# Optimization experiments

Hardware: AMD Instinct MI355X
Metric: run time of the kernel (lower is better)

The kernel has to match this reference:

```python
import jax, jax.numpy as jnp
import jax.scipy.linalg as jsl
import numpy as np

B, T, C = 2, 4096, 1024
HK = HV = 8           # linear_num_key_heads == linear_num_value_heads
DK = DV = 128         # linear_key_head_dim / linear_value_head_dim
CHUNK = 64
CONV_K = 4
KEY_DIM = HK * DK
VAL_DIM = HV * DV
CONV_DIM = 2 * KEY_DIM + VAL_DIM
EPS = 1e-6


def setup_inputs() -> dict:
    key = jax.random.key(0)
    ks = jax.random.split(key, 8)
    s = 0.02
    x = jax.random.normal(ks[0], (B, T, C), jnp.float32)
    W_qkvz = jax.random.normal(ks[1], (C, 2 * KEY_DIM + 2 * VAL_DIM), jnp.float32) * s
    W_ba = jax.random.normal(ks[2], (C, 2 * HV), jnp.float32) * s
    conv_w = jax.random.normal(ks[3], (CONV_DIM, 1, CONV_K), jnp.float32) * 0.3  # depthwise (O,1,K)
    dt_bias = jnp.ones((HV,), jnp.float32)
    A_log = jnp.log(jax.random.uniform(ks[4], (HV,), jnp.float32, 0.5, 8.0))
    norm_weight = jnp.ones((DV,), jnp.float32)
    W_out = jax.random.normal(ks[5], (VAL_DIM, C), jnp.float32) * s
    return {"x": x, "W_qkvz": W_qkvz, "W_ba": W_ba, "conv_w": conv_w,
            "dt_bias": dt_bias, "A_log": A_log, "norm_weight": norm_weight, "W_out": W_out}


def _l2norm(x, eps=EPS):
    return x * jax.lax.rsqrt(jnp.sum(x * x, -1, keepdims=True) + eps)


def _chunk_gated_delta_rule(q, k, v, g, beta, chunk=CHUNK):
    # q,k: (B,T,H,DK); v: (B,T,H,DV); g,beta: (B,T,H)
    q = _l2norm(q)
    k = _l2norm(k)
    tr = lambda x: jnp.swapaxes(x, 1, 2).astype(jnp.float32)  # -> (B,H,T,...)
    q, k, v, g, beta = tr(q), tr(k), tr(v), tr(g), tr(beta)
    b, h, t, dk = k.shape
    dv = v.shape[-1]
    n = t // chunk  # T divisible by chunk (pad_size == 0)
    q = q * (dk ** -0.5)
    v_beta = v * beta[..., None]
    k_beta = k * beta[..., None]
    rs = lambda x: x.reshape(b, h, n, chunk, x.shape[-1])
    q, k, v_beta, k_beta = rs(q), rs(k), rs(v_beta), rs(k_beta)
    g = jnp.cumsum(g.reshape(b, h, n, chunk), axis=-1)
    # decay_mask[..., i, j] = exp(g_i - g_j) for j <= i, else 0
    decay = jnp.tril(jnp.exp(jnp.tril(g[..., :, None] - g[..., None, :])))
    # forward substitution == unit-lower-triangular solve: (I + tri)^{-1}
    tri = jnp.tril(jnp.einsum('bhnck,bhndk->bhncd', k_beta, k) * decay, -1)
    eye = jnp.eye(chunk, dtype=jnp.float32)
    Tm = jsl.solve_triangular(eye + tri, jnp.broadcast_to(eye, tri.shape), lower=True)
    v_new = Tm @ v_beta                                   # (B,H,N,C,DV)
    k_cum = Tm @ (k_beta * jnp.exp(g)[..., None])         # (B,H,N,C,DK)
    keep_low = jnp.tril(jnp.ones((chunk, chunk), bool))

    def step(S, inp):
        q_i, k_i, v_i, kc_i, g_i, dm_i = inp              # (B,H,C,*)
        attn = jnp.where(keep_low, (q_i @ jnp.swapaxes(k_i, -1, -2)) * dm_i, 0.0)
        v_n = v_i - kc_i @ S
        out = (q_i * jnp.exp(g_i)[..., None]) @ S + attn @ v_n
        g_last = g_i[..., -1]
        S = S * jnp.exp(g_last)[..., None, None] + jnp.einsum(
            'bhck,bhcv->bhkv', k_i * jnp.exp(g_last[..., None] - g_i)[..., None], v_n)
        return S, out

    mv = lambda x: jnp.moveaxis(x, 2, 0)                  # chunk axis to front
    S0 = jnp.zeros((b, h, dk, dv), jnp.float32)
    S, outs = jax.lax.scan(step, S0, (mv(q), mv(k), mv(v_new), mv(k_cum), mv(g), mv(decay)))
    out = jnp.moveaxis(outs, 0, 2).reshape(b, h, t, dv)
    return jnp.swapaxes(out, 1, 2), S                     # (B,T,H,DV), (B,H,DK,DV)


def reference(x, W_qkvz, W_ba, conv_w, dt_bias, A_log, norm_weight, W_out):
    Bx, Tx, Cx = x.shape
    ratio = HV // HK
    qkvz = (x @ W_qkvz).reshape(Bx, Tx, HK, 2 * DK + 2 * ratio * DV)
    q, k, v, z = jnp.split(qkvz, [DK, 2 * DK, 2 * DK + ratio * DV], axis=3)
    v = v.reshape(Bx, Tx, HV, DV)
    z = z.reshape(Bx, Tx, HV, DV)
    ba = (x @ W_ba).reshape(Bx, Tx, HK, 2 * ratio)
    b_, a_ = jnp.split(ba, [ratio], axis=3)
    b_ = b_.reshape(Bx, Tx, HV)
    a_ = a_.reshape(Bx, Tx, HV)
    mixed = jnp.concatenate([q.reshape(Bx, Tx, -1), k.reshape(Bx, Tx, -1),
                             v.reshape(Bx, Tx, -1)], axis=-1)
    # causal depthwise conv1d (left pad K-1, take first T)
    xc = jnp.swapaxes(mixed, 1, 2)                        # (B, CONV_DIM, T)
    conv = jax.lax.conv_general_dilated(xc, conv_w, (1,), [(CONV_K - 1, 0)],
                                        dimension_numbers=('NCH', 'OIH', 'NCH'),
                                        feature_group_count=CONV_DIM)
    conv = jnp.swapaxes(jax.nn.silu(conv), 1, 2)          # (B,T,CONV_DIM)
    qc, kc, vc = jnp.split(conv, [KEY_DIM, 2 * KEY_DIM], axis=-1)
    qc = qc.reshape(Bx, Tx, HK, DK)
    kc = kc.reshape(Bx, Tx, HK, DK)
    vc = vc.reshape(Bx, Tx, HV, DV)
    if ratio > 1:
        qc = jnp.repeat(qc, ratio, axis=2)
        kc = jnp.repeat(kc, ratio, axis=2)
    beta = jax.nn.sigmoid(b_)
    g = -jnp.exp(A_log) * jax.nn.softplus(a_ + dt_bias)
    core, _ = _chunk_gated_delta_rule(qc, kc, vc, g, beta)
    # GatedRMSNorm over head_v_dim, gated by silu(z)
    h = core.astype(jnp.float32)
    var = jnp.mean(h * h, -1, keepdims=True)
    h = norm_weight * (h * jax.lax.rsqrt(var + EPS))
    h = h * jax.nn.silu(z.astype(jnp.float32))
    return h.reshape(Bx, Tx, VAL_DIM) @ W_out
```

## Files before the change

kernel.cpp:

```cpp
#include <hip/hip_runtime.h>
#include <cstddef>

#define Bx 2
#define Tn 4096
#define Hh 8

typedef unsigned short u16;
typedef unsigned int u32;
typedef __attribute__((ext_vector_type(8))) short short8;
typedef __attribute__((ext_vector_type(4))) float f32x4;

__device__ __forceinline__ float bf2f(u16 u) {
  u32 x = ((u32)u) << 16;
  return __uint_as_float(x);
}
__device__ __forceinline__ u16 f2bf(float f) {
  u32 x = __float_as_uint(f);
  u32 lsb = (x >> 16) & 1;
  x += 0x7fffu + lsb;
  return (u16)(x >> 16);
}
__device__ __forceinline__ u32 pack2(float a, float b) {
  return (u32)f2bf(a) | ((u32)f2bf(b) << 16);
}
__device__ __forceinline__ short8 cvt8(float4 f0, float4 f1) {
  uint4 p;
  p.x = pack2(f0.x, f0.y);
  p.y = pack2(f0.z, f0.w);
  p.z = pack2(f1.x, f1.y);
  p.w = pack2(f1.z, f1.w);
  return *(short8*)&p;
}
__device__ __forceinline__ void async16(u16* lds, const u16* g) {
  __builtin_amdgcn_global_load_lds((const __attribute__((address_space(1))) void*)g,
                                   (__attribute__((address_space(3))) void*)lds, 16, 0, 0);
}

__global__ __launch_bounds__(256) void conv_bf16(const float* __restrict__ X,
                                                 u16* __restrict__ Xb) {
  int i = (blockIdx.x * 256 + threadIdx.x) * 8;
  float4 v0 = *(const float4*)&X[i];
  float4 v1 = *(const float4*)&X[i + 4];
  uint4 pv;
  pv.x = pack2(v0.x, v0.y);
  pv.y = pack2(v0.z, v0.w);
  pv.z = pack2(v1.x, v1.y);
  pv.w = pack2(v1.z, v1.w);
  *(uint4*)&Xb[i] = pv;
}

__global__ __launch_bounds__(256) void transpose_bf16(const float* __restrict__ W,
                                                      u16* __restrict__ WT,
                                                      int K, int N) {
  __shared__ float tile[64][68];
  int nb = blockIdx.x, kb = blockIdx.y;
  int tid = threadIdx.x;
  int r = tid >> 4, c4 = (tid & 15) * 4;
#pragma unroll
  for (int p = 0; p < 4; p++) {
    int k = kb * 64 + p * 16 + r;
    float4 v = *(const float4*)&W[(size_t)k * N + nb * 64 + c4];
    tile[p * 16 + r][c4] = v.x;
    tile[p * 16 + r][c4 + 1] = v.y;
    tile[p * 16 + r][c4 + 2] = v.z;
    tile[p * 16 + r][c4 + 3] = v.w;
  }
  __syncthreads();
  int rn = tid >> 2, ck = (tid & 3) * 16;
#pragma unroll
  for (int s = 0; s < 2; s++) {
    int k0 = ck + s * 8;
    uint4 pv;
    pv.x = pack2(tile[k0 + 0][rn], tile[k0 + 1][rn]);
    pv.y = pack2(tile[k0 + 2][rn], tile[k0 + 3][rn]);
    pv.z = pack2(tile[k0 + 4][rn], tile[k0 + 5][rn]);
    pv.w = pack2(tile[k0 + 6][rn], tile[k0 + 7][rn]);
    *(uint4*)&WT[(size_t)(nb * 64 + rn) * K + kb * 64 + k0] = pv;
  }
}

template<int EPI>
__global__ __launch_bounds__(256) void gemm_mfma(const u16* __restrict__ A,
                                                 const u16* __restrict__ Bt,
                                                 u16* __restrict__ O1,
                                                 u16* __restrict__ O2,
                                                 float* __restrict__ O3,
                                                 int Nfull) {
  const int K = 1024;
  __shared__ u16 As[128 * 64];
  __shared__ u16 Bs[128 * 64];
  int lin = blockIdx.y * gridDim.x + blockIdx.x;
  int sl = lin >> 3;
  int cbn = gridDim.x >> 3;
  int bn = (lin & 7) * cbn + (sl % cbn);
  int bm = sl / cbn;
  int tid = threadIdx.x;
  int wave = tid >> 6, lane = tid & 63;
  int wr = wave >> 1, wc = wave & 1;

  f32x4 acc[4][4];
#pragma unroll
  for (int i = 0; i < 4; i++)
#pragma unroll
    for (int j = 0; j < 4; j++) acc[i][j] = (f32x4){0.f, 0.f, 0.f, 0.f};

  int srow = lane >> 3;
  int gc8 = ((lane & 7) ^ srow) * 8;
  const u16* Ab = A + (size_t)(bm * 128 + wave * 32 + srow) * K + gc8;
  const u16* Bb = Bt + (size_t)(bn * 128 + wave * 32 + srow) * K + gc8;
  u16* AsW = &As[(wave * 32) * 64];
  u16* BsW = &Bs[(wave * 32) * 64];

  int m_lane = lane & 15, kgrp = lane >> 4;
  int m7 = m_lane & 7;

  for (int kk = 0; kk < K; kk += 64) {
    __syncthreads();
#pragma unroll
    for (int i = 0; i < 4; i++) {
      async16(AsW + i * 512, Ab + (size_t)(i * 8) * K + kk);
      async16(BsW + i * 512, Bb + (size_t)(i * 8) * K + kk);
    }
    __syncthreads();
    short8 a[4][2], b[4][2];
#pragma unroll
    for (int t = 0; t < 4; t++)
#pragma unroll
      for (int ks = 0; ks < 2; ks++) {
        a[t][ks] = *(const short8*)&As[(wr * 64 + t * 16 + m_lane) * 64 +
                                       (((ks * 4 + kgrp) ^ m7) << 3)];
        b[t][ks] = *(const short8*)&Bs[(wc * 64 + t * 16 + m_lane) * 64 +
                                       (((ks * 4 + kgrp) ^ m7) << 3)];
      }
#pragma unroll
    for (int ks = 0; ks < 2; ks++)
#pragma unroll
      for (int i = 0; i < 4; i++)
#pragma unroll
        for (int j = 0; j < 4; j++)
          acc[i][j] = __builtin_amdgcn_mfma_f32_16x16x32_bf16(a[i][ks], b[j][ks],
                                                              acc[i][j], 0, 0, 0);
  }

  int n0 = bn * 128;
  int cbase = wc * 64 + (lane & 15);
  int rbase = bm * 128 + wr * 64 + ((lane >> 4) * 4);
  if (EPI == 1) {
    int h = n0 >> 9, sub = (n0 >> 7) & 3;
    u16* dst;
    size_t stride;
    if (sub < 3) { dst = O1 + (size_t)(sub * 1024 + h * 128); stride = 3072; }
    else         { dst = O2 + (size_t)(h * 128);              stride = 1024; }
#pragma unroll
    for (int i = 0; i < 4; i++)
#pragma unroll
      for (int j = 0; j < 4; j++)
#pragma unroll
        for (int r = 0; r < 4; r++)
          dst[(size_t)(rbase + i * 16 + r) * stride + cbase + j * 16] = f2bf(acc[i][j][r]);
  } else {
#pragma unroll
    for (int i = 0; i < 4; i++)
#pragma unroll
      for (int j = 0; j < 4; j++)
#pragma unroll
        for (int r = 0; r < 4; r++)
          O3[(size_t)(rbase + i * 16 + r) * Nfull + n0 + cbase + j * 16] = acc[i][j][r];
  }
}

__global__ __launch_bounds__(128) void ba_kernel(const float* __restrict__ x,
                                                 const float* __restrict__ Wba,
                                                 const float* __restrict__ dtb,
                                                 const float* __restrict__ Alog,
                                                 float* __restrict__ betab,
                                                 float* __restrict__ gb) {
  __shared__ float xs[1024];
  __shared__ float part[8][16];
  int row = blockIdx.x, tid = threadIdx.x;
#pragma unroll
  for (int r = 0; r < 2; r++) {
    int f4 = r * 128 + tid;
    *(float4*)&xs[f4 * 4] = *(const float4*)&x[(size_t)row * 1024 + f4 * 4];
  }
  __syncthreads();
  int col = tid & 15, seg = tid >> 4;
  float a = 0.f;
  for (int k = seg * 128; k < seg * 128 + 128; k++) a += xs[k] * Wba[k * 16 + col];
  part[seg][col] = a;
  __syncthreads();
  if (tid < 8) {
    float bval = 0.f, aval = 0.f;
#pragma unroll
    for (int q = 0; q < 8; q++) { bval += part[q][tid * 2]; aval += part[q][tid * 2 + 1]; }
    betab[(size_t)row * 8 + tid] = 1.f / (1.f + expf(-bval));
    float spin = aval + dtb[tid];
    float sp = (spin > 20.f) ? spin : log1pf(expf(spin));
    gb[(size_t)row * 8 + tid] = -expf(Alog[tid]) * sp;
  }
}

__global__ __launch_bounds__(256) void convnorm(const u16* __restrict__ mixed,
                                                const float* __restrict__ cw,
                                                const float* __restrict__ gbuf,
                                                u16* __restrict__ qn,
                                                u16* __restrict__ kn,
                                                u16* __restrict__ kdT) {
  __shared__ __align__(16) u16 sRaw[67 * 128];
  __shared__ __align__(16) u16 sO[64 * 136];
  __shared__ float red_s[256];
  __shared__ float inv_s[64];
  __shared__ float eglc_s[64];
  int n = blockIdx.x, bh = blockIdx.y, type = blockIdx.z;
  int b = bh >> 3, h = bh & 7;
  int t0 = n * 64, tid = threadIdx.x;
  int srow = tid >> 4, scol8 = (tid & 15) * 8;
  int base = type * 1024;

#pragma unroll
  for (int pass = 0; pass < 5; pass++) {
    int r = pass * 16 + srow;
    if (r < 67) {
      int t = t0 - 3 + r;
      uint4 v = make_uint4(0u, 0u, 0u, 0u);
      if (t >= 0) v = *(const uint4*)&mixed[(size_t)(b * Tn + t) * 3072 + base + h * 128 + scol8];
      *(uint4*)&sRaw[r * 128 + scol8] = v;
    }
  }
  if (type == 1 && tid < 64) {
    float gv = gbuf[(size_t)(b * Tn + t0 + tid) * 8 + h];
#pragma unroll
    for (int off = 1; off < 64; off <<= 1) {
      float o = __shfl_up(gv, off, 64);
      if (tid >= off) gv += o;
    }
    float gl = __shfl(gv, 63, 64);
    eglc_s[tid] = expf(gl - gv);
  }
  __syncthreads();

#pragma unroll
  for (int it = 0; it < 32; it++) {
    int idx = it * 256 + tid;
    int i = idx >> 7, d = idx & 127;
    int colw = (base + h * 128 + d) * 4;
    float a = 0.f;
#pragma unroll
    for (int tap = 0; tap < 4; tap++)
      a += bf2f(sRaw[(i + tap) * 128 + d]) * cw[colw + tap];
    a = a / (1.f + expf(-a));
    sO[i * 136 + d] = f2bf(a);
  }
  __syncthreads();
  {
    int i = tid >> 2, p = tid & 3;
    float ss = 0.f;
#pragma unroll
    for (int d = p * 32; d < p * 32 + 32; d += 2) {
      u32 w2 = *(const u32*)&sO[i * 136 + d];
      float a = bf2f(w2 & 0xffff), b2 = bf2f(w2 >> 16);
      ss += a * a + b2 * b2;
    }
    red_s[tid] = ss;
  }
  __syncthreads();
  if (tid < 64) {
    float inv = rsqrtf(red_s[tid * 4] + red_s[tid * 4 + 1] + red_s[tid * 4 + 2] + red_s[tid * 4 + 3] + 1e-6f);
    inv_s[tid] = (type == 0) ? inv * 0.08838834764831845f : inv;
  }
  __syncthreads();
  u16* dstRow = (type == 0 ? qn : kn) + (size_t)(bh * Tn + t0) * 128;
#pragma unroll
  for (int it = 0; it < 16; it++) {
    int idx = it * 256 + tid;
    int i = idx >> 6, d2 = (idx & 63) * 2;
    u32 w2 = *(const u32*)&sO[i * 136 + d2];
    float inv = inv_s[i];
    float q0 = bf2f(w2 & 0xffff) * inv, q1 = bf2f(w2 >> 16) * inv;
    u32 pk = pack2(q0, q1);
    if (type == 1) *(u32*)&sO[i * 136 + d2] = pk;
    *(u32*)&dstRow[(size_t)i * 128 + d2] = pk;
  }
  if (type == 1) {
    __syncthreads();
    const size_t tbase = (size_t)(bh * 64 + n) * 8192;
#pragma unroll
    for (int it = 0; it < 32; it++) {
      int idx = it * 256 + tid;
      int d = idx >> 6, i = idx & 63;
      kdT[tbase + d * 64 + i] = f2bf(bf2f(sO[i * 136 + d]) * eglc_s[i]);
    }
  }
}

__global__ __launch_bounds__(256) void prep(const u16* __restrict__ mixed,
                                            const float* __restrict__ cw,
                                            const float* __restrict__ gbuf,
                                            const float* __restrict__ betabuf,
                                            u16* qbuf,
                                            u16* kbuf,
                                            u16* __restrict__ vnT,
                                            u16* __restrict__ attn,
                                            float* __restrict__ egl) {
  __shared__ __align__(16) u16 sKn[64 * 136];
  __shared__ __align__(16) u16 sQn[64 * 136];
  __shared__ __align__(16) u16 sRawV[67 * 128];
  __shared__ float gc_s[64], egc_s[64], bet_s[64];
  float* triL = (float*)sQn;

  int n = blockIdx.x, bh = blockIdx.y;
  int b = bh >> 3, h = bh & 7;
  int t0 = n * 64;
  int tid = threadIdx.x;
  const int rowg0 = b * Tn + t0;
  const int rowh0 = bh * Tn + t0;
  const size_t tbase = (size_t)(bh * 64 + n) * 8192;

  int wv = tid >> 6, lane = tid & 63;
  int m16 = lane & 15, q8 = (lane >> 4) * 8, qr = (lane >> 4) * 4;
  int srow = tid >> 4, scol8 = (tid & 15) * 8;

#pragma unroll
  for (int it = 0; it < 4; it++) {
    int idx = it * 256 + tid;
    int i = idx >> 4, c8 = (idx & 15) * 8;
    *(uint4*)&sQn[i * 136 + c8] = *(const uint4*)&qbuf[(size_t)(rowh0 + i) * 128 + c8];
    *(uint4*)&sKn[i * 136 + c8] = *(const uint4*)&kbuf[(size_t)(rowh0 + i) * 128 + c8];
  }
#pragma unroll
  for (int pass = 0; pass < 5; pass++) {
    int r = pass * 16 + srow;
    if (r < 67) {
      int t = t0 - 3 + r;
      uint4 v = make_uint4(0u, 0u, 0u, 0u);
      if (t >= 0) v = *(const uint4*)&mixed[(size_t)(b * Tn + t) * 3072 + 2048 + h * 128 + scol8];
      *(uint4*)&sRawV[r * 128 + scol8] = v;
    }
  }
  if (tid < 64) {
    float gv = gbuf[(size_t)(rowg0 + tid) * 8 + h];
    float bv = betabuf[(size_t)(rowg0 + tid) * 8 + h];
#pragma unroll
    for (int off = 1; off < 64; off <<= 1) {
      float o = __shfl_up(gv, off, 64);
      if (tid >= off) gv += o;
    }
    float gl = __shfl(gv, 63, 64);
    gc_s[tid] = gv;
    egc_s[tid] = expf(gv);
    bet_s[tid] = bv;
    if (tid == 63) egl[bh * 64 + n] = expf(gl);
  }
  __syncthreads();

#pragma unroll
  for (int it = 0; it < 16; it++) {
    int idx = it * 256 + tid;
    int i = idx >> 6, d2 = (idx & 63) * 2;
    u32 w2 = *(const u32*)&sQn[i * 136 + d2];
    float e = egc_s[i];
    *(u32*)&qbuf[(size_t)(rowh0 + i) * 128 + d2] =
        pack2(bf2f(w2 & 0xffff) * e, bf2f(w2 >> 16) * e);
  }
  {
    short8 qa[4];
#pragma unroll
    for (int kt = 0; kt < 4; kt++)
      qa[kt] = *(const short8*)&sQn[(wv * 16 + m16) * 136 + kt * 32 + q8];
    u16* atp = attn + (size_t)(bh * 64 + n) * 4096;
#pragma unroll
    for (int jt = 0; jt < 4; jt++) {
      int j = jt * 16 + m16;
      if (jt <= wv) {
        f32x4 o = (f32x4){0.f, 0.f, 0.f, 0.f};
#pragma unroll
        for (int kt = 0; kt < 4; kt++) {
          short8 kb = *(const short8*)&sKn[(jt * 16 + m16) * 136 + kt * 32 + q8];
          o = __builtin_amdgcn_mfma_f32_16x16x32_bf16(qa[kt], kb, o, 0, 0, 0);
        }
#pragma unroll
        for (int r = 0; r < 4; r++) {
          int i = wv * 16 + qr + r;
          float val = (j <= i) ? o[r] * expf(gc_s[i] - gc_s[j]) : 0.f;
          atp[i * 64 + j] = f2bf(val);
        }
      } else {
#pragma unroll
        for (int r = 0; r < 4; r++) atp[(wv * 16 + qr + r) * 64 + j] = 0;
      }
    }
  }
  __syncthreads();
  {
    short8 ka[4];
#pragma unroll
    for (int kt = 0; kt < 4; kt++)
      ka[kt] = *(const short8*)&sKn[(wv * 16 + m16) * 136 + kt * 32 + q8];
#pragma unroll
    for (int jt = 0; jt < 4; jt++) {
      int j = jt * 16 + m16;
      if (jt <= wv) {
        f32x4 o = (f32x4){0.f, 0.f, 0.f, 0.f};
#pragma unroll
        for (int kt = 0; kt < 4; kt++) {
          short8 kb = *(const short8*)&sKn[(jt * 16 + m16) * 136 + kt * 32 + q8];
          o = __builtin_amdgcn_mfma_f32_16x16x32_bf16(ka[kt], kb, o, 0, 0, 0);
        }
#pragma unroll
        for (int r = 0; r < 4; r++) {
          int i = wv * 16 + qr + r;
          triL[i * 64 + j] = (j < i) ? bet_s[i] * expf(gc_s[i] - gc_s[j]) * o[r] : 0.f;
        }
      } else if (jt == wv + 1) {
#pragma unroll
        for (int r = 0; r < 4; r++) triL[(wv * 16 + qr + r) * 64 + j] = 0.f;
      }
    }
  }
  __syncthreads();

  {
    int mat = tid >> 7, c = tid & 127;
    float x[64];
    if (mat == 0) {
#pragma unroll
      for (int i = 0; i < 64; i++)
        x[i] = bf2f(sKn[i * 136 + c]) * bet_s[i] * egc_s[i];
    } else {
      float cwv[4];
      int colw = (2048 + h * 128 + c) * 4;
#pragma unroll
      for (int tap = 0; tap < 4; tap++) cwv[tap] = cw[colw + tap];
#pragma unroll
      for (int i = 0; i < 64; i++) {
        float a = 0.f;
#pragma unroll
        for (int tap = 0; tap < 4; tap++)
          a += bf2f(sRawV[(i + tap) * 128 + c]) * cwv[tap];
        a = a / (1.f + expf(-a));
        x[i] = a * bet_s[i];
      }
    }
#pragma unroll
    for (int i = 1; i < 64; i++) {
      float s0 = 0.f, s1 = 0.f, s2 = 0.f, s3 = 0.f;
#pragma unroll
      for (int l4 = 0; l4 < (i + 3) / 4; l4++) {
        float4 t4 = *(float4*)&triL[i * 64 + l4 * 4];
        s0 += t4.x * x[l4 * 4 + 0];
        s1 += t4.y * x[l4 * 4 + 1];
        s2 += t4.z * x[l4 * 4 + 2];
        s3 += t4.w * x[l4 * 4 + 3];
      }
      x[i] = x[i] - ((s0 + s1) + (s2 + s3));
    }
    if (mat == 0) {
#pragma unroll
      for (int i = 0; i < 64; i++) kbuf[(size_t)(rowh0 + i) * 128 + c] = f2bf(-x[i]);
    } else {
#pragma unroll
      for (int i = 0; i < 64; i += 2)
        *(u32*)&vnT[tbase + c * 64 + i] = pack2(x[i], x[i + 1]);
    }
  }
}

__device__ __forceinline__ void stage_quarter(int w, u16* ldsb,
                                              const u16* __restrict__ qgc,
                                              const u16* __restrict__ kcc,
                                              const u16* __restrict__ ktc,
                                              const u16* __restrict__ atc,
                                              const u16* __restrict__ vtc,
                                              int lane) {
  int l8 = lane * 8;
  if (w == 0) {
#pragma unroll
    for (int i = 0; i < 16; i++) {
      int p = i * 512 + l8;
      async16(ldsb + 8192 + i * 512, kcc + (p ^ ((((p >> 7) & 15)) << 3)));
    }
  } else if (w == 1) {
#pragma unroll
    for (int i = 0; i < 16; i++) {
      int p = i * 512 + l8;
      async16(ldsb + 16384 + i * 512, ktc + (p ^ ((((p >> 6) & 7)) << 3)));
    }
  } else if (w == 2) {
#pragma unroll
    for (int i = 0; i < 16; i++) {
      int p = i * 512 + l8;
      async16(ldsb + i * 512, qgc + (p ^ ((((p >> 7) & 15)) << 3)));
    }
  } else {
#pragma unroll
    for (int i = 0; i < 8; i++) {
      int p = i * 512 + l8;
      async16(ldsb + 24576 + i * 512, atc + (p ^ ((((p >> 6) & 7)) << 3)));
    }
#pragma unroll
    for (int i = 0; i < 2; i++) {
      int p = i * 512 + l8;
      async16(ldsb + 28672 + i * 512, vtc + (p ^ ((((p >> 6) & 7)) << 3)));
    }
  }
}

__global__ __launch_bounds__(256, 1) void scan_mfma(const u16* __restrict__ qg,
                                                    const u16* __restrict__ kdT,
                                                    const u16* __restrict__ vnT,
                                                    const u16* __restrict__ kcum,
                                                    const u16* __restrict__ attn,
                                                    const float* __restrict__ egl,
                                                    float* __restrict__ core) {
  extern __shared__ __align__(16) u16 dyn[];
  __shared__ __align__(16) u16 STb[16 * 128];
  __shared__ __align__(16) u16 VNb[16 * 64];
  int blk = blockIdx.x;
  int bh = blk & 15, tile = blk >> 4;
  int dv0 = tile * 16;
  int b = bh >> 3, h = bh & 7;
  int tid = threadIdx.x;
  int w = tid >> 6, lane = tid & 63;
  int q = lane >> 4, col = lane & 15;
  int c7 = col & 7;
  int qh = q >> 1, ql = q & 1;

  for (int r = tid; r < 16 * 128 / 2; r += 256) ((u32*)STb)[r] = 0u;
  float egAll = egl[bh * 64 + lane];

  f32x4 st0 = (f32x4){0.f, 0.f, 0.f, 0.f};
  f32x4 st1 = (f32x4){0.f, 0.f, 0.f, 0.f};

  const u16* qg_base = qg + (size_t)bh * Tn * 128;
  const u16* kc_base = kcum + (size_t)bh * Tn * 128;
  const u16* kt_base = kdT + (size_t)bh * 64 * 8192;
  const u16* at_base = attn + (size_t)bh * 64 * 4096;
  const u16* vt_base = vnT + (size_t)bh * 64 * 8192 + dv0 * 64;

  stage_quarter(w, dyn, qg_base, kc_base, kt_base, at_base, vt_base, lane);
  asm volatile("s_waitcnt vmcnt(0)" ::: "memory");
  __syncthreads();

  for (int n = 0; n < 64; n++) {
    u16* buf = dyn + (n & 1) * 29696;

    short8 kcf[4], qgf[4], ktf[4], atf[2], sb[4];
    uint2 vtf;
#pragma unroll
    for (int kt = 0; kt < 4; kt++) {
      kcf[kt] = *(const short8*)&buf[8192 + (w * 16 + col) * 128 + (((kt * 4 + q) ^ col) << 3)];
      qgf[kt] = *(const short8*)&buf[(w * 16 + col) * 128 + (((kt * 4 + q) ^ col) << 3)];
      sb[kt] = *(const short8*)&STb[col * 128 + (((kt * 4 + q) ^ col) << 3)];
    }
#pragma unroll
    for (int kt2 = 0; kt2 < 2; kt2++) {
      atf[kt2] = *(const short8*)&buf[24576 + (w * 16 + col) * 64 + (((kt2 * 4 + q) ^ c7) << 3)];
#pragma unroll
      for (int t = 0; t < 2; t++)
        ktf[t * 2 + kt2] = *(const short8*)&buf[16384 + ((w * 2 + t) * 16 + col) * 64 +
                                                (((kt2 * 4 + q) ^ c7) << 3)];
    }
    vtf = *(const uint2*)&buf[28672 + col * 64 + (((w * 2 + qh) ^ c7) << 3) + ql * 4];

    if (n < 63) {
      stage_quarter(w, dyn + ((n + 1) & 1) * 29696,
                    qg_base + (size_t)(n + 1) * 8192,
                    kc_base + (size_t)(n + 1) * 8192,
                    kt_base + (size_t)(n + 1) * 8192,
                    at_base + (size_t)(n + 1) * 4096,
                    vt_base + (size_t)(n + 1) * 8192, lane);
    }
    float eg = __shfl(egAll, n, 64);

    {
      f32x4 a0;
      a0[0] = bf2f(vtf.x & 0xffff); a0[1] = bf2f(vtf.x >> 16);
      a0[2] = bf2f(vtf.y & 0xffff); a0[3] = bf2f(vtf.y >> 16);
#pragma unroll
      for (int kt = 0; kt < 4; kt++)
        a0 = __builtin_amdgcn_mfma_f32_16x16x32_bf16(kcf[kt], sb[kt], a0, 0, 0, 0);
      uint2 pk;
      pk.x = pack2(a0[0], a0[1]);
      pk.y = pack2(a0[2], a0[3]);
      *(uint2*)&VNb[col * 64 + (((w * 2 + qh) ^ c7) << 3) + ql * 4] = pk;
    }
    asm volatile("s_waitcnt lgkmcnt(0)" ::: "memory");
    __builtin_amdgcn_s_barrier();
    __builtin_amdgcn_sched_barrier(0);

    short8 vb[2];
#pragma unroll
    for (int kt2 = 0; kt2 < 2; kt2++)
      vb[kt2] = *(const short8*)&VNb[col * 64 + (((kt2 * 4 + q) ^ c7) << 3)];

    {
      f32x4 s0;
      s0[0] = st0[0] * eg; s0[1] = st0[1] * eg; s0[2] = st0[2] * eg; s0[3] = st0[3] * eg;
      s0 = __builtin_amdgcn_mfma_f32_16x16x32_bf16(ktf[0], vb[0], s0, 0, 0, 0);
      s0 = __builtin_amdgcn_mfma_f32_16x16x32_bf16(ktf[1], vb[1], s0, 0, 0, 0);
      st0 = s0;
      uint2 pk;
      pk.x = pack2(s0[0], s0[1]);
      pk.y = pack2(s0[2], s0[3]);
      *(uint2*)&STb[col * 128 + ((((w * 2 + 0) * 2 + qh) ^ col) << 3) + ql * 4] = pk;
    }
    {
      f32x4 s1;
      s1[0] = st1[0] * eg; s1[1] = st1[1] * eg; s1[2] = st1[2] * eg; s1[3] = st1[3] * eg;
      s1 = __builtin_amdgcn_mfma_f32_16x16x32_bf16(ktf[2], vb[0], s1, 0, 0, 0);
      s1 = __builtin_amdgcn_mfma_f32_16x16x32_bf16(ktf[3], vb[1], s1, 0, 0, 0);
      st1 = s1;
      uint2 pk;
      pk.x = pack2(s1[0], s1[1]);
      pk.y = pack2(s1[2], s1[3]);
      *(uint2*)&STb[col * 128 + ((((w * 2 + 1) * 2 + qh) ^ col) << 3) + ql * 4] = pk;
    }

    {
      f32x4 o = (f32x4){0.f, 0.f, 0.f, 0.f};
#pragma unroll
      for (int kt = 0; kt < 4; kt++)
        o = __builtin_amdgcn_mfma_f32_16x16x32_bf16(qgf[kt], sb[kt], o, 0, 0, 0);
#pragma unroll
      for (int kt2 = 0; kt2 < 2; kt2++)
        o = __builtin_amdgcn_mfma_f32_16x16x32_bf16(atf[kt2], vb[kt2], o, 0, 0, 0);
      size_t rowb = (size_t)(b * Tn) + n * 64 + w * 16 + q * 4;
#pragma unroll
      for (int r2 = 0; r2 < 4; r2++)
        core[(rowb + r2) * 1024 + h * 128 + dv0 + col] = o[r2];
    }

    asm volatile("s_waitcnt vmcnt(4) lgkmcnt(0)" ::: "memory");
    __builtin_amdgcn_s_barrier();
    __builtin_amdgcn_sched_barrier(0);
  }
}

__global__ __launch_bounds__(256) void gnorm(const float* __restrict__ core,
                                             const u16* __restrict__ z,
                                             const float* __restrict__ nw,
                                             u16* __restrict__ coreb) {
  __shared__ float red[256];
  __shared__ float rstd[8];
  int row = blockIdx.x, tid = threadIdx.x;
  float4 c4 = *(const float4*)&core[(size_t)row * 1024 + tid * 4];
  uint2 zl = *(const uint2*)&z[(size_t)row * 1024 + tid * 4];
  float4 z4;
  z4.x = bf2f(zl.x & 0xffff); z4.y = bf2f(zl.x >> 16);
  z4.z = bf2f(zl.y & 0xffff); z4.w = bf2f(zl.y >> 16);
  red[tid] = c4.x * c4.x + c4.y * c4.y + c4.z * c4.z + c4.w * c4.w;
  __syncthreads();
  if (tid < 8) {
    float s = 0.f;
    for (int t2 = tid * 32; t2 < tid * 32 + 32; t2++) s += red[t2];
    rstd[tid] = rsqrtf(s * (1.f / 128.f) + 1e-6f);
  }
  __syncthreads();
  float rs = rstd[tid >> 5];
  int d0 = (tid * 4) & 127;
  float4 w4 = *(const float4*)&nw[d0];
  float4 o;
  o.x = c4.x * rs * w4.x * (z4.x / (1.f + expf(-z4.x)));
  o.y = c4.y * rs * w4.y * (z4.y / (1.f + expf(-z4.y)));
  o.z = c4.z * rs * w4.z * (z4.z / (1.f + expf(-z4.z)));
  o.w = c4.w * rs * w4.w * (z4.w / (1.f + expf(-z4.w)));
  uint2 pv;
  pv.x = pack2(o.x, o.y);
  pv.y = pack2(o.z, o.w);
  *(uint2*)&coreb[(size_t)row * 1024 + tid * 4] = pv;
}

extern "C" void kernel_launch(void* const* d_in, const int* in_sizes, int n_in,
                              void* d_out, int out_size, void* d_ws, size_t ws_size,
                              hipStream_t stream) {
  const float* x     = (const float*)d_in[0];
  const float* Wqkvz = (const float*)d_in[1];
  const float* Wba   = (const float*)d_in[2];
  const float* convw = (const float*)d_in[3];
  const float* dtb   = (const float*)d_in[4];
  const float* Alog  = (const float*)d_in[5];
  const float* nw    = (const float*)d_in[6];
  const float* Wout  = (const float*)d_in[7];
  float* out = (float*)d_out;

  char* w = (char*)d_ws;
  u16*   mixed = (u16*)w;
  float* core  = (float*)w;
  u16*   coreb = (u16*)(w + 33554432);
  u16*   zb    = (u16*)(w + 50331648);
  float* betab = (float*)(w + 67108864);
  float* gb    = (float*)(w + 67371008);
  u16*   qgB   = (u16*)(w + 67633152);
  u16*   xb    = (u16*)(w + 67633152);
  u16*   kdTB  = (u16*)(w + 84410368);
  u16*   WqT   = (u16*)(w + 84410368);
  u16*   vnTB  = (u16*)(w + 101187584);
  u16*   kcB   = (u16*)(w + 117964800);
  u16*   WoT   = (u16*)(w + 117964800);
  u16*   atB   = (u16*)(w + 134742016);
  float* eglB  = (float*)(w + 143130624);

  static bool attr_set = false;
  if (!attr_set) {
    hipFuncSetAttribute(reinterpret_cast<const void*>(scan_mfma),
                        hipFuncAttributeMaxDynamicSharedMemorySize, 118784);
    attr_set = true;
  }

  conv_bf16<<<dim3(4096), 256, 0, stream>>>(x, xb);
  transpose_bf16<<<dim3(64, 16), 256, 0, stream>>>(Wqkvz, WqT, 1024, 4096);
  gemm_mfma<1><<<dim3(32, 64), 256, 0, stream>>>(xb, WqT, mixed, zb, nullptr, 4096);
  ba_kernel<<<dim3(8192), 128, 0, stream>>>(x, Wba, dtb, Alog, betab, gb);
  convnorm<<<dim3(64, 16, 2), 256, 0, stream>>>(mixed, convw, gb, qgB, kcB, kdTB);
  prep<<<dim3(64, 16), 256, 0, stream>>>(mixed, convw, gb, betab, qgB, kcB, vnTB, atB, eglB);
  scan_mfma<<<dim3(128), 256, 118784, stream>>>(qgB, kdTB, vnTB, kcB, atB, eglB, core);
  transpose_bf16<<<dim3(16, 16), 256, 0, stream>>>(Wout, WoT, 1024, 1024);
  gnorm<<<dim3(8192), 256, 0, stream>>>(core, zb, nw, coreb);
  gemm_mfma<0><<<dim3(8, 64), 256, 0, stream>>>(coreb, WoT, nullptr, nullptr, out, 1024);
}
```

Before: 400.3 us.

## Add dedicated 256x256-tile double-buffered async GEMM for QKVZ projection

Replaces the generic 128x128 MFMA GEMM for the input projection with a specialized kernel that uses 256x256 output tiles, 512 threads, and a double-buffered shared-memory pipeline fed by async global-to-LDS loads with XOR swizzling. Larger tiles raise arithmetic intensity and reduce global traffic, and overlapping the next K-slice load with MFMA compute hides memory latency. In exchange it uses 128 KB of LDS and many accumulator registers, limiting occupancy to one block per CU, and stores outputs element-wise with strided bf16 writes.

```diff
diff --git a/kernel.cpp b/kernel.cpp
--- a/kernel.cpp
+++ b/kernel.cpp
@@ -77,6 +77,97 @@
     pv.w = pack2(tile[k0 + 6][rn], tile[k0 + 7][rn]);
     *(uint4*)&WT[(size_t)(nb * 64 + rn) * K + kb * 64 + k0] = pv;
   }
+}
+
+__global__ __launch_bounds__(512, 1) void gemm_qkvz(const u16* __restrict__ A,
+                                                    const u16* __restrict__ Bt,
+                                                    u16* __restrict__ O1,
+                                                    u16* __restrict__ O2) {
+  const int K = 1024;
+  extern __shared__ __align__(16) u16 gl[];
+  int lin = blockIdx.x;
+  int sl = (lin & 7) * 64 + (lin >> 3);
+  int bm = sl & 31;
+  int bn = sl >> 5;
+  int tid = threadIdx.x;
+  int wid = tid >> 6, lane = tid & 63;
+  int wm = wid >> 2, wn = wid & 3;
+  int m_lane = lane & 15, kgrp = lane >> 4, m7 = m_lane & 7;
+
+  f32x4 acc[8][4];
+#pragma unroll
+  for (int i = 0; i < 8; i++)
+#pragma unroll
+    for (int j = 0; j < 4; j++) acc[i][j] = (f32x4){0.f, 0.f, 0.f, 0.f};
+
+  int srow = lane >> 3;
+  int gc8 = ((lane & 7) ^ srow) * 8;
+  const u16* Ab = A + (size_t)(bm * 256 + wid * 32 + srow) * K + gc8;
+  const u16* Bb = Bt + (size_t)(bn * 256 + wid * 32 + srow) * K + gc8;
+
+#pragma unroll
+  for (int i = 0; i < 4; i++) {
+    async16(gl + (wid * 32 + i * 8) * 64, Ab + (size_t)(i * 8) * K);
+    async16(gl + 32768 + (wid * 32 + i * 8) * 64, Bb + (size_t)(i * 8) * K);
+  }
+  asm volatile("s_waitcnt vmcnt(0)" ::: "memory");
+  __builtin_amdgcn_s_barrier();
+
+  for (int t = 0; t < 16; t++) {
+    int p = t & 1;
+    const u16* Ap = gl + p * 16384;
+    const u16* Bp = gl + 32768 + p * 16384;
+    if (t < 15) {
+      int pn = p ^ 1;
+      int kk = (t + 1) * 64;
+#pragma unroll
+      for (int i = 0; i < 4; i++) {
+        async16(gl + pn * 16384 + (wid * 32 + i * 8) * 64, Ab + (size_t)(i * 8) * K + kk);
+        async16(gl + 32768 + pn * 16384 + (wid * 32 + i * 8) * 64, Bb + (size_t)(i * 8) * K + kk);
+      }
+    }
+    short8 bq[2][4];
+#pragma unroll
+    for (int ks = 0; ks < 2; ks++)
+#pragma unroll
+      for (int nf = 0; nf < 4; nf++)
+        bq[ks][nf] = *(const short8*)&Bp[(wn * 64 + nf * 16 + m_lane) * 64 +
+                                         (((ks * 4 + kgrp) ^ m7) << 3)];
+#pragma unroll
+    for (int mf = 0; mf < 8; mf++) {
+      short8 aq0 = *(const short8*)&Ap[(wm * 128 + mf * 16 + m_lane) * 64 +
+                                       ((kgrp ^ m7) << 3)];
+      short8 aq1 = *(const short8*)&Ap[(wm * 128 + mf * 16 + m_lane) * 64 +
+                                       (((4 + kgrp) ^ m7) << 3)];
+#pragma unroll
+      for (int nf = 0; nf < 4; nf++)
+        acc[mf][nf] = __builtin_amdgcn_mfma_f32_16x16x32_bf16(aq0, bq[0][nf], acc[mf][nf], 0, 0, 0);
+#pragma unroll
+      for (int nf = 0; nf < 4; nf++)
+        acc[mf][nf] = __builtin_amdgcn_mfma_f32_16x16x32_bf16(aq1, bq[1][nf], acc[mf][nf], 0, 0, 0);
+    }
+    if (t < 15) {
+      asm volatile("s_waitcnt vmcnt(0) lgkmcnt(0)" ::: "memory");
+      __builtin_amdgcn_s_barrier();
+      __builtin_amdgcn_sched_barrier(0);
+    }
+  }
+
+  int n0w = bn * 256 + wn * 64;
+  int h = n0w >> 9, sub = (n0w >> 7) & 3;
+  int cin = ((n0w & 127) & 64) + m_lane;
+  u16* dst;
+  size_t stride;
+  if (sub < 3) { dst = O1 + (size_t)(sub * 1024 + h * 128); stride = 3072; }
+  else         { dst = O2 + (size_t)(h * 128);              stride = 1024; }
+  int rbase = bm * 256 + wm * 128 + kgrp * 4;
+#pragma unroll
+  for (int mf = 0; mf < 8; mf++)
+#pragma unroll
+    for (int nf = 0; nf < 4; nf++)
+#pragma unroll
+      for (int r = 0; r < 4; r++)
+        dst[(size_t)(rbase + mf * 16 + r) * stride + cin + nf * 16] = f2bf(acc[mf][nf][r]);
 }
 
 template<int EPI>
@@ -704,12 +795,14 @@
   if (!attr_set) {
     hipFuncSetAttribute(reinterpret_cast<const void*>(scan_mfma),
                         hipFuncAttributeMaxDynamicSharedMemorySize, 118784);
+    hipFuncSetAttribute(reinterpret_cast<const void*>(gemm_qkvz),
+                        hipFuncAttributeMaxDynamicSharedMemorySize, 131072);
     attr_set = true;
   }
 
   conv_bf16<<<dim3(4096), 256, 0, stream>>>(x, xb);
   transpose_bf16<<<dim3(64, 16), 256, 0, stream>>>(Wqkvz, WqT, 1024, 4096);
-  gemm_mfma<1><<<dim3(32, 64), 256, 0, stream>>>(xb, WqT, mixed, zb, nullptr, 4096);
+  gemm_qkvz<<<dim3(512), 512, 131072, stream>>>(xb, WqT, mixed, zb);
   ba_kernel<<<dim3(8192), 128, 0, stream>>>(x, Wba, dtb, Alog, betab, gb);
   convnorm<<<dim3(64, 16, 2), 256, 0, stream>>>(mixed, convw, gb, qgB, kcB, kdTB);
   prep<<<dim3(64, 16), 256, 0, stream>>>(mixed, convw, gb, betab, qgB, kcB, vnTB, atB, eglB);
```

Result: no change. 396.9 us (-0.8%).
